# Performance work log

Measured on AMD Instinct MI355X. Metric: run time of the kernel, lower is better.

Reference implementation:

```python
import jax, jax.numpy as jnp
import numpy as np

D_MODEL, D_FF, N_EXPERTS, TOP_K = 1024, 4096, 4, 2
B, S = 4, 2048


def setup_inputs() -> dict:
    key = jax.random.key(0)
    ks = jax.random.split(key, 7)
    s_r = 1.0 / np.sqrt(D_MODEL)
    s_f = 1.0 / np.sqrt(D_FF)
    return {
        "x": jax.random.normal(ks[0], (B, S, D_MODEL), dtype=jnp.float32),
        "Wr": jax.random.uniform(ks[1], (D_MODEL, N_EXPERTS), jnp.float32, -s_r, s_r),
        "br": jnp.zeros((N_EXPERTS,), jnp.float32),
        "W1": jax.random.uniform(ks[2], (N_EXPERTS, D_MODEL, D_FF), jnp.float32, -s_r, s_r),
        "b1": jax.random.uniform(ks[3], (N_EXPERTS, D_FF), jnp.float32, -s_r, s_r),
        "W2": jax.random.uniform(ks[4], (N_EXPERTS, D_FF, D_MODEL), jnp.float32, -s_f, s_f),
        "b2": jax.random.uniform(ks[5], (N_EXPERTS, D_MODEL), jnp.float32, -s_f, s_f),
    }


def reference(x, Wr, br, W1, b1, W2, b2):
    # Router: (B,S,E)
    router_logits = jnp.einsum("bsd,de->bse", x, Wr) + br
    router_probs = jax.nn.softmax(router_logits, axis=-1)
    top_k_probs, top_k_idx = jax.lax.top_k(router_probs, TOP_K)  # (B,S,K)
    top_k_probs = top_k_probs / jnp.sum(top_k_probs, axis=-1, keepdims=True)

    # Dense all-experts compute (faithful to original module).
    h = jnp.einsum("bsd,edf->bsef", x, W1) + b1          # (B,S,E,F)
    h = jax.nn.gelu(h, approximate=False)                 # torch nn.GELU (erf)
    expert_out = jnp.einsum("bsef,efd->bsed", h, W2) + b2  # (B,S,E,D)

    # Gather top-k expert outputs and combine with renormalized probs.
    sel = jnp.take_along_axis(expert_out, top_k_idx[..., None], axis=2)  # (B,S,K,D)
    out = jnp.sum(sel * top_k_probs[..., None], axis=2)   # (B,S,D)
    return out
```

## Files before the change

### kernel.cpp

```cpp
#include <hip/hip_runtime.h>
#include <hip/hip_bf16.h>
#include <hip/hip_fp16.h>
#include <stdint.h>

typedef float    f32x4 __attribute__((ext_vector_type(4)));
typedef float    fvec4 __attribute__((ext_vector_type(4)));
typedef _Float16 f16x8 __attribute__((ext_vector_type(8)));

#define D_MODEL 1024
#define D_FF    4096
#define NTOK    8192
#define CAP_ROWS 16896
#define NRB      132

#define OFF_W1  0UL
#define OFF_W2  33554432UL
#define OFF_XG  67108864UL
#define OFF_H   101711872UL
#define OFF_CNT 240123904UL
#define OFF_OFS 240123936UL
#define OFF_TOK 240124160UL
#define OFF_E12 240259328UL
#define OFF_W12 240292096UL
#define WS_NEED 240357632UL

__device__ __forceinline__ void gload_lds16(const void* g, void* l) {
  __builtin_amdgcn_global_load_lds(
      (const __attribute__((address_space(1))) unsigned int*)g,
      (__attribute__((address_space(3))) unsigned int*)l, 16, 0, 0);
}

__device__ __forceinline__ float fast_gelu(float v) {
  float v2 = v * v;
  float y2 = v * (2.302118131f + 0.10293924f * v2);
  float t = exp2f(y2);
  return v - v * __builtin_amdgcn_rcpf(1.f + t);
}

__device__ __forceinline__ void wtrans_body(
    const float* __restrict__ in, _Float16* __restrict__ out,
    int K, int N, int e, int n0, int k0, float (*tile)[65]) {
  const float* src = in + (size_t)e * K * N;
  _Float16* dst = out + (size_t)e * K * N;
  int t = threadIdx.x;
  {
    int kk = t >> 2, nc = (t & 3) * 16;
    const float* p = src + (size_t)(k0 + kk) * N + n0 + nc;
#pragma unroll
    for (int j = 0; j < 4; ++j) {
      fvec4 v = *(const fvec4*)(p + j * 4);
      tile[kk][nc + j * 4 + 0] = v[0]; tile[kk][nc + j * 4 + 1] = v[1];
      tile[kk][nc + j * 4 + 2] = v[2]; tile[kk][nc + j * 4 + 3] = v[3];
    }
  }
  __syncthreads();
  {
    int nn = t >> 2, kb = (t & 3) * 16;
    f16x8 o0, o1;
#pragma unroll
    for (int j = 0; j < 8; ++j) o0[j] = (_Float16)tile[kb + j][nn];
#pragma unroll
    for (int j = 0; j < 8; ++j) o1[j] = (_Float16)tile[kb + 8 + j][nn];
    _Float16* q = dst + (size_t)(n0 + nn) * K + k0 + kb;
    *(f16x8*)q = o0;
    *((f16x8*)q + 1) = o1;
  }
}

__global__ __launch_bounds__(256) void rwc_k(
    const float* __restrict__ x, const float* __restrict__ Wr,
    const float* __restrict__ br, int* __restrict__ e12,
    float* __restrict__ w12,
    const float* __restrict__ W1, _Float16* __restrict__ W1f,
    _Float16* __restrict__ x16) {
  __shared__ float tile[64][65];
  int b = blockIdx.x;
  if (b >= 6144) {
    int row = (b - 6144) * 2 + (threadIdx.x >> 7);
    int tid = threadIdx.x & 127;
    const float* src = x + (size_t)row * D_MODEL + tid * 8;
    fvec4 v0 = *(const fvec4*)src;
    fvec4 v1 = *(const fvec4*)(src + 4);
    f16x8 o;
#pragma unroll
    for (int j = 0; j < 4; ++j) { o[j] = (_Float16)v0[j]; o[4 + j] = (_Float16)v1[j]; }
    *(f16x8*)(x16 + (size_t)row * D_MODEL + tid * 8) = o;
    return;
  }
  if (b >= 2048) {
    int bb = b - 2048;
    int n0 = (bb & 63) * 64, k0 = ((bb >> 6) & 15) * 64, e = bb >> 10;
    wtrans_body(W1, W1f, 1024, 4096, e, n0, k0, tile);
    return;
  }
  int wid = threadIdx.x >> 6, lane = threadIdx.x & 63;
  int t = b * 4 + wid;
  const float* xr = x + (size_t)t * D_MODEL;
  float a0 = 0.f, a1 = 0.f, a2 = 0.f, a3 = 0.f;
#pragma unroll
  for (int c = 0; c < 4; ++c) {
    int d0 = c * 256 + lane * 4;
    fvec4 xv = *(const fvec4*)(xr + d0);
#pragma unroll
    for (int j = 0; j < 4; ++j) {
      fvec4 wv = *(const fvec4*)(Wr + (size_t)(d0 + j) * 4);
      a0 += xv[j] * wv[0]; a1 += xv[j] * wv[1];
      a2 += xv[j] * wv[2]; a3 += xv[j] * wv[3];
    }
  }
#pragma unroll
  for (int m = 32; m; m >>= 1) {
    a0 += __shfl_xor(a0, m, 64); a1 += __shfl_xor(a1, m, 64);
    a2 += __shfl_xor(a2, m, 64); a3 += __shfl_xor(a3, m, 64);
  }
  if (lane == 0) {
    float l[4] = {a0 + br[0], a1 + br[1], a2 + br[2], a3 + br[3]};
    int e1 = 0; float m1 = l[0];
#pragma unroll
    for (int e = 1; e < 4; ++e) if (l[e] > m1) { m1 = l[e]; e1 = e; }
    int e2 = -1; float m2 = -1e30f;
#pragma unroll
    for (int e = 0; e < 4; ++e) if (e != e1 && l[e] > m2) { m2 = l[e]; e2 = e; }
    float tt = expf(m2 - m1);
    float w1 = 1.f / (1.f + tt), w2 = tt / (1.f + tt);
    e12[t] = e1 | (e2 << 8);
    w12[2 * t] = w1; w12[2 * t + 1] = w2;
  }
}

__global__ __launch_bounds__(256) void plan_k(
    int* __restrict__ e12, const float* __restrict__ w12,
    int* __restrict__ counts, int* __restrict__ offs,
    int* __restrict__ tok) {
  __shared__ int ls[4][256];
  __shared__ int lt[4];
  __shared__ int lo[5];
  int tid = threadIdx.x;
  int t0 = tid * 32;
  int pe[32];
  int c0 = 0, c1 = 0, c2 = 0, c3 = 0;
#pragma unroll
  for (int j = 0; j < 32; ++j) {
    int p = e12[t0 + j];
    pe[j] = p;
    int e1 = p & 255, e2 = p >> 8;
    c0 += (e1 == 0) + (e2 == 0);
    c1 += (e1 == 1) + (e2 == 1);
    c2 += (e1 == 2) + (e2 == 2);
    c3 += (e1 == 3) + (e2 == 3);
  }
  ls[0][tid] = c0; ls[1][tid] = c1; ls[2][tid] = c2; ls[3][tid] = c3;
  __syncthreads();
  int wv = tid >> 6, lane = tid & 63;
  {
    int s0 = ls[wv][lane * 4 + 0], s1 = ls[wv][lane * 4 + 1];
    int s2 = ls[wv][lane * 4 + 2], s3 = ls[wv][lane * 4 + 3];
    int s = s0 + s1 + s2 + s3;
    int incl = s;
#pragma unroll
    for (int d = 1; d < 64; d <<= 1) {
      int tsh = __shfl_up(incl, d, 64);
      if (lane >= d) incl += tsh;
    }
    int excl = incl - s;
    ls[wv][lane * 4 + 0] = excl;
    ls[wv][lane * 4 + 1] = excl + s0;
    ls[wv][lane * 4 + 2] = excl + s0 + s1;
    ls[wv][lane * 4 + 3] = excl + s0 + s1 + s2;
    if (lane == 63) lt[wv] = incl;
  }
  __syncthreads();
  if (tid == 0) {
    int o = 0;
#pragma unroll
    for (int e = 0; e < 4; ++e) {
      lo[e] = o; offs[e] = o; counts[e] = lt[e];
      o += (lt[e] + 127) & ~127;
    }
    lo[4] = o; offs[4] = o;
  }
  __syncthreads();
  int b0 = lo[0] + ls[0][tid], b1 = lo[1] + ls[1][tid];
  int b2 = lo[2] + ls[2][tid], b3 = lo[3] + ls[3][tid];
#pragma unroll
  for (int j = 0; j < 32; ++j) {
    int p = pe[j];
    int t = t0 + j;
    int e1 = p & 255, e2 = p >> 8;
    int s1 = (e1 == 0) ? b0 : (e1 == 1) ? b1 : (e1 == 2) ? b2 : b3;
    tok[s1] = t;
    b0 += (e1 == 0); b1 += (e1 == 1); b2 += (e1 == 2); b3 += (e1 == 3);
    int s2 = (e2 == 0) ? b0 : (e2 == 1) ? b1 : (e2 == 2) ? b2 : b3;
    tok[s2] = t;
    b0 += (e2 == 0); b1 += (e2 == 1); b2 += (e2 == 2); b3 += (e2 == 3);
    e12[t] = s1 | (s2 << 16);
  }
#pragma unroll
  for (int e = 0; e < 4; ++e) {
    int start = lo[e] + lt[e];
    int end = lo[e + 1];
    for (int i = start + tid; i < end; i += 256) tok[i] = 0;
  }
}

__device__ __forceinline__ f16x8 lds_frag(const char* base, int row, int kbyte) {
  return *(const f16x8*)(base + row * 128 + (kbyte ^ ((row & 7) << 4)));
}

__global__ __launch_bounds__(256, 2) void gemm1x_k(
    const _Float16* __restrict__ x16, const _Float16* __restrict__ B,
    const float* __restrict__ bias, const int* __restrict__ offs,
    const int* __restrict__ counts, const int* __restrict__ tok,
    _Float16* __restrict__ outH,
    const float* __restrict__ W2, _Float16* __restrict__ W2f) {
  __shared__ char lds[49152];
  int bid = blockIdx.x;
  if (bid >= 2112) {
    int bb = bid - 2112;
    int n0 = (bb & 15) * 64, k0 = ((bb >> 4) & 63) * 64, e = bb >> 10;
    wtrans_body(W2, W2f, 4096, 1024, e, n0, k0, (float(*)[65])lds);
    return;
  }
  int wg = (bid & 7) * 264 + (bid >> 3);
  int col = wg & 15, row = wg >> 4;
  int rowBase = row * 128;
  if (rowBase >= offs[4]) return;
  int e = 0;
  while (e < 3 && rowBase >= offs[e + 1]) ++e;
  if (rowBase >= offs[e] + counts[e]) return;
  int colBase = col * 256;

  int tid = threadIdx.x, wid = tid >> 6, lane = tid & 63;
  int wr = wid >> 1, wc = wid & 1;
  int ln = lane & 15;
  int srow = lane >> 3;
  int kx = (lane & 7) ^ srow;
  const _Float16* Asrc[4];
#pragma unroll
  for (int i = 0; i < 4; ++i) {
    int tk = tok[rowBase + (wid * 4 + i) * 8 + srow];
    Asrc[i] = x16 + (size_t)tk * 1024 + kx * 8;
  }
  const _Float16* Bbase = B + (size_t)e * D_FF * 1024 + (size_t)colBase * 1024 + kx * 8;
  char* ldsA = lds;
  char* ldsB = lds + 16384;

  f32x4 acc[4][8];
  f32x4 zero = {0.f, 0.f, 0.f, 0.f};
#pragma unroll
  for (int m = 0; m < 4; ++m)
#pragma unroll
    for (int n = 0; n < 8; ++n) acc[m][n] = zero;

  for (int k0 = 0; k0 < 1024; k0 += 64) {
#pragma unroll
    for (int i = 0; i < 4; ++i) {
      int chunk = wid * 4 + i;
      gload_lds16(Asrc[i] + k0, ldsA + chunk * 1024);
    }
#pragma unroll
    for (int i = 0; i < 8; ++i) {
      int chunk = wid * 8 + i;
      gload_lds16(Bbase + (size_t)(chunk * 8 + srow) * 1024 + k0, ldsB + chunk * 1024);
    }
    __syncthreads();
#pragma unroll
    for (int kk = 0; kk < 2; ++kk) {
      int kbyte = kk * 64 + (lane >> 4) * 16;
      f16x8 af[4], bf[8];
#pragma unroll
      for (int m = 0; m < 4; ++m)
        af[m] = lds_frag(ldsA, wr * 64 + m * 16 + ln, kbyte);
#pragma unroll
      for (int n = 0; n < 8; ++n)
        bf[n] = lds_frag(ldsB, wc * 128 + n * 16 + ln, kbyte);
#pragma unroll
      for (int m = 0; m < 4; ++m)
#pragma unroll
        for (int n = 0; n < 8; ++n)
          acc[m][n] = __builtin_amdgcn_mfma_f32_16x16x32_f16(af[m], bf[n], acc[m][n], 0, 0, 0);
    }
    __syncthreads();
  }

  int col0 = colBase + wc * 128 + ln;
  float bv[8];
#pragma unroll
  for (int n = 0; n < 8; ++n) bv[n] = bias[(size_t)e * D_FF + col0 + n * 16];
#pragma unroll
  for (int m = 0; m < 4; ++m) {
    int rbase = rowBase + wr * 64 + m * 16 + (lane >> 4) * 4;
#pragma unroll
    for (int j = 0; j < 4; ++j) {
      size_t ro = (size_t)(rbase + j) * D_FF;
#pragma unroll
      for (int n = 0; n < 8; ++n) {
        float v = fast_gelu(acc[m][n][j] + bv[n]);
        outH[ro + col0 + n * 16] = (_Float16)v;
      }
    }
  }
}

__global__ __launch_bounds__(256, 4) void gemm2_k(
    const _Float16* __restrict__ A, const _Float16* __restrict__ B,
    const float* __restrict__ bias, const int* __restrict__ offs,
    const int* __restrict__ counts, _Float16* __restrict__ Eout) {
  __shared__ char lds[32768];
  int bid = blockIdx.x;
  int wg = (bid & 7) * 132 + (bid >> 3);
  int col = wg & 7, row = wg >> 3;
  int rowBase = row * 128;
  if (rowBase >= offs[4]) return;
  int e = 0;
  while (e < 3 && rowBase >= offs[e + 1]) ++e;
  int eoff = offs[e], cnt = counts[e];
  if (rowBase >= eoff + cnt) return;
  int colBase = col * 128;

  int tid = threadIdx.x, wid = tid >> 6, lane = tid & 63;
  int wr = wid >> 1, wc = wid & 1;
  int ln = lane & 15;
  int srow = lane >> 3;
  int kx = (lane & 7) ^ srow;
  const _Float16* Abase = A + (size_t)rowBase * 4096 + kx * 8;
  const _Float16* Bbase = B + (size_t)e * D_MODEL * 4096 + (size_t)colBase * 4096 + kx * 8;
  char* ldsA = lds;
  char* ldsB = lds + 16384;

  f32x4 acc[4][4];
  f32x4 zero = {0.f, 0.f, 0.f, 0.f};
#pragma unroll
  for (int m = 0; m < 4; ++m)
#pragma unroll
    for (int n = 0; n < 4; ++n) acc[m][n] = zero;

  for (int k0 = 0; k0 < 4096; k0 += 64) {
#pragma unroll
    for (int i = 0; i < 4; ++i) {
      int chunk = wid * 4 + i;
      gload_lds16(Abase + (size_t)(chunk * 8 + srow) * 4096 + k0, ldsA + chunk * 1024);
      gload_lds16(Bbase + (size_t)(chunk * 8 + srow) * 4096 + k0, ldsB + chunk * 1024);
    }
    __syncthreads();
#pragma unroll
    for (int kk = 0; kk < 2; ++kk) {
      int kbyte = kk * 64 + (lane >> 4) * 16;
      f16x8 af[4], bf[4];
#pragma unroll
      for (int m = 0; m < 4; ++m)
        af[m] = lds_frag(ldsA, wr * 64 + m * 16 + ln, kbyte);
#pragma unroll
      for (int n = 0; n < 4; ++n)
        bf[n] = lds_frag(ldsB, wc * 64 + n * 16 + ln, kbyte);
#pragma unroll
      for (int m = 0; m < 4; ++m)
#pragma unroll
        for (int n = 0; n < 4; ++n)
          acc[m][n] = __builtin_amdgcn_mfma_f32_16x16x32_f16(af[m], bf[n], acc[m][n], 0, 0, 0);
    }
    __syncthreads();
  }

  int col0 = colBase + wc * 64 + ln;
  float bv[4];
#pragma unroll
  for (int n = 0; n < 4; ++n) bv[n] = bias[(size_t)e * D_MODEL + col0 + n * 16];
#pragma unroll
  for (int m = 0; m < 4; ++m) {
    int rbase = rowBase + wr * 64 + m * 16 + (lane >> 4) * 4;
#pragma unroll
    for (int j = 0; j < 4; ++j) {
      int grow = rbase + j;
      if (grow - eoff < cnt) {
        size_t o = (size_t)grow * D_MODEL + col0;
#pragma unroll
        for (int n = 0; n < 4; ++n)
          Eout[o + n * 16] = (_Float16)(acc[m][n][j] + bv[n]);
      }
    }
  }
}

__global__ __launch_bounds__(256) void combine_k(
    const _Float16* __restrict__ Eout, const int* __restrict__ sl12,
    const float* __restrict__ w12, float* __restrict__ out) {
  int t = blockIdx.x * 2 + (threadIdx.x >> 7);
  int tid = threadIdx.x & 127;
  int p = sl12[t];
  int s1 = p & 0xffff, s2 = (p >> 16) & 0xffff;
  float w1 = w12[2 * t], w2 = w12[2 * t + 1];
  f16x8 a = *(const f16x8*)(Eout + (size_t)s1 * D_MODEL + tid * 8);
  f16x8 b = *(const f16x8*)(Eout + (size_t)s2 * D_MODEL + tid * 8);
  fvec4 o0, o1;
#pragma unroll
  for (int j = 0; j < 4; ++j) {
    o0[j] = w1 * (float)a[j] + w2 * (float)b[j];
    o1[j] = w1 * (float)a[4 + j] + w2 * (float)b[4 + j];
  }
  float* dst = out + (size_t)t * D_MODEL + tid * 8;
  *(fvec4*)dst = o0;
  *(fvec4*)(dst + 4) = o1;
}

extern "C" void kernel_launch(void* const* d_in, const int* in_sizes, int n_in,
                              void* d_out, int out_size, void* d_ws, size_t ws_size,
                              hipStream_t stream) {
  const float* x  = (const float*)d_in[0];
  const float* Wr = (const float*)d_in[1];
  const float* br = (const float*)d_in[2];
  const float* W1 = (const float*)d_in[3];
  const float* b1 = (const float*)d_in[4];
  const float* W2 = (const float*)d_in[5];
  const float* b2 = (const float*)d_in[6];
  float* out = (float*)d_out;
  char* ws = (char*)d_ws;
  if (ws_size < WS_NEED) return;

  _Float16* W1f = (_Float16*)(ws + OFF_W1);
  _Float16* W2f = (_Float16*)(ws + OFF_W2);
  _Float16* x16 = (_Float16*)(ws + OFF_XG);
  _Float16* H   = (_Float16*)(ws + OFF_H);
  int*   counts = (int*)(ws + OFF_CNT);
  int*   offs   = (int*)(ws + OFF_OFS);
  int*   tok    = (int*)(ws + OFF_TOK);
  int*   e12    = (int*)(ws + OFF_E12);
  float* w12    = (float*)(ws + OFF_W12);
  _Float16* Eout = x16;

  rwc_k<<<10240, 256, 0, stream>>>(x, Wr, br, e12, w12, W1, W1f, x16);
  plan_k<<<1, 256, 0, stream>>>(e12, w12, counts, offs, tok);
  gemm1x_k<<<6208, 256, 0, stream>>>(x16, W1f, b1, offs, counts, tok, H, W2, W2f);
  gemm2_k<<<NRB * 8, 256, 0, stream>>>(H, W2f, b2, offs, counts, Eout);
  combine_k<<<NTOK / 2, 256, 0, stream>>>(Eout, e12, w12, out);
}
```

Before: 446.0 us.

## Double-buffer LDS in gemm2 with manual waitcnt and MFMA priority

Turns the gemm2 main loop into a two-stage LDS ping-pong. The tile for step t+2 is issued right after step t's compute, and the loop waits only until the older stage's loads land (vmcnt(8)) rather than draining all loads each step. It also raises wave priority around the MFMA block and doubles the LDS to 64KB with launch bounds lowered to 2 blocks per CU. The aim is to hide global load latency behind compute, at the cost of occupancy. The last iterations redundantly reload tile 63.

```diff
diff --git a/kernel.cpp b/kernel.cpp
--- a/kernel.cpp
+++ b/kernel.cpp
@@ -302,11 +302,15 @@
   }
 }
 
-__global__ __launch_bounds__(256, 4) void gemm2_k(
+#define G2BAR  asm volatile("s_barrier" ::: "memory")
+#define G2VM8  asm volatile("s_waitcnt vmcnt(8)" ::: "memory")
+#define G2LGKM asm volatile("s_waitcnt lgkmcnt(0)" ::: "memory")
+
+__global__ __launch_bounds__(256, 2) void gemm2_k(
     const _Float16* __restrict__ A, const _Float16* __restrict__ B,
     const float* __restrict__ bias, const int* __restrict__ offs,
     const int* __restrict__ counts, _Float16* __restrict__ Eout) {
-  __shared__ char lds[32768];
+  __shared__ char lds[65536];
   int bid = blockIdx.x;
   int wg = (bid & 7) * 132 + (bid >> 3);
   int col = wg & 7, row = wg >> 3;
@@ -325,8 +329,6 @@
   int kx = (lane & 7) ^ srow;
   const _Float16* Abase = A + (size_t)rowBase * 4096 + kx * 8;
   const _Float16* Bbase = B + (size_t)e * D_MODEL * 4096 + (size_t)colBase * 4096 + kx * 8;
-  char* ldsA = lds;
-  char* ldsB = lds + 16384;
 
   f32x4 acc[4][4];
   f32x4 zero = {0.f, 0.f, 0.f, 0.f};
@@ -335,32 +337,50 @@
 #pragma unroll
     for (int n = 0; n < 4; ++n) acc[m][n] = zero;
 
-  for (int k0 = 0; k0 < 4096; k0 += 64) {
+  auto STAGE = [&](int kt, int b) {
+    char* lA = lds + (b << 15);
+    char* lB = lA + 16384;
+    int k0 = kt * 64;
 #pragma unroll
     for (int i = 0; i < 4; ++i) {
       int chunk = wid * 4 + i;
-      gload_lds16(Abase + (size_t)(chunk * 8 + srow) * 4096 + k0, ldsA + chunk * 1024);
-      gload_lds16(Bbase + (size_t)(chunk * 8 + srow) * 4096 + k0, ldsB + chunk * 1024);
-    }
-    __syncthreads();
+      gload_lds16(Abase + (size_t)(chunk * 8 + srow) * 4096 + k0, lA + chunk * 1024);
+      gload_lds16(Bbase + (size_t)(chunk * 8 + srow) * 4096 + k0, lB + chunk * 1024);
+    }
+  };
+
+  STAGE(0, 0);
+  STAGE(1, 1);
+
+  for (int t = 0; t < 64; ++t) {
+    G2VM8;
+    G2BAR;
+    const char* cA = lds + ((t & 1) << 15);
+    const char* cB = cA + 16384;
 #pragma unroll
     for (int kk = 0; kk < 2; ++kk) {
       int kbyte = kk * 64 + (lane >> 4) * 16;
       f16x8 af[4], bf[4];
 #pragma unroll
       for (int m = 0; m < 4; ++m)
-        af[m] = lds_frag(ldsA, wr * 64 + m * 16 + ln, kbyte);
+        af[m] = lds_frag(cA, wr * 64 + m * 16 + ln, kbyte);
 #pragma unroll
       for (int n = 0; n < 4; ++n)
-        bf[n] = lds_frag(ldsB, wc * 64 + n * 16 + ln, kbyte);
+        bf[n] = lds_frag(cB, wc * 64 + n * 16 + ln, kbyte);
+      G2LGKM;
+      __builtin_amdgcn_s_setprio(1);
 #pragma unroll
       for (int m = 0; m < 4; ++m)
 #pragma unroll
         for (int n = 0; n < 4; ++n)
           acc[m][n] = __builtin_amdgcn_mfma_f32_16x16x32_f16(af[m], bf[n], acc[m][n], 0, 0, 0);
-    }
-    __syncthreads();
-  }
+      __builtin_amdgcn_s_setprio(0);
+    }
+    G2BAR;
+    int tn = t + 2; if (tn > 63) tn = 63;
+    STAGE(tn, t & 1);
+  }
+  asm volatile("s_waitcnt vmcnt(0)" ::: "memory");
 
   int col0 = colBase + wc * 64 + ln;
   float bv[4];
```

After: 439.2 us. About the same (-1.5%).
